# Kernel optimization log

Measured on AMD Instinct MI355X. Metric: run time of the kernel, lower is better.

The kernel has to match this reference:

```python
import jax, jax.numpy as jnp
import numpy as np

B, L, D, NL, VOCAB = 2, 8192, 512, 8, 32
FFT_LEN = 2 * L  # causal linear conv via zero-padded FFT


def layernorm(x, g, b, eps=1e-5):
    mu = jnp.mean(x, axis=-1, keepdims=True)
    var = jnp.var(x, axis=-1, keepdims=True)
    return (x - mu) * jax.lax.rsqrt(var + eps) * g + b


def fftconv(v, h, bias):
    # v: [B, d, L], h: [d, L] long implicit filter, bias: [d] skip (the Hyena 'D' term)
    vf = jnp.fft.rfft(v, n=FFT_LEN)
    hf = jnp.fft.rfft(h, n=FFT_LEN)
    y = jnp.fft.irfft(vf * hf[None], n=FFT_LEN)[..., :L]
    return y + v * bias[:, None]


def short_conv(p, w, b):
    # causal depthwise conv, kernel size 3: p [B, C, L], w [C, 3], b [C]
    pp = jnp.pad(p, ((0, 0), (0, 0), (2, 0)))
    out = jax.lax.conv_general_dilated(pp, w[:, None, :], (1,), 'VALID',
                                       feature_group_count=p.shape[1])
    return out + b[None, :, None]


def setup_inputs() -> dict:
    key = jax.random.key(0)
    ks = jax.random.split(key, 12)
    rn = lambda k, sh, s: jax.random.normal(k, sh, jnp.float32) * s
    d = D
    return {
        'input_ids': jax.random.randint(ks[0], (B, L), 0, VOCAB),
        'emb': rn(ks[1], (VOCAB, d), 0.02),
        'ln1_g': jnp.ones((NL, d)), 'ln1_b': jnp.zeros((NL, d)),
        'Win': rn(ks[2], (NL, d, 3 * d), d ** -0.5), 'bin_': jnp.zeros((NL, 3 * d)),
        'convw': rn(ks[3], (NL, 3 * d, 3), 3 ** -0.5), 'convb': jnp.zeros((NL, 3 * d)),
        'h': rn(ks[4], (NL, d, L), L ** -0.5),  # implicit long filter, materialized
        'Db': rn(ks[5], (NL, d), 1.0),
        'Wout': rn(ks[6], (NL, d, d), d ** -0.5), 'bout': jnp.zeros((NL, d)),
        'ln2_g': jnp.ones((NL, d)), 'ln2_b': jnp.zeros((NL, d)),
        'W1': rn(ks[7], (NL, d, 4 * d), d ** -0.5), 'b1': jnp.zeros((NL, 4 * d)),
        'W2': rn(ks[8], (NL, 4 * d, d), (4 * d) ** -0.5), 'b2': jnp.zeros((NL, d)),
        'lnf_g': jnp.ones((d,)), 'lnf_b': jnp.zeros((d,)),
    }


def reference(input_ids, emb, ln1_g, ln1_b, Win, bin_, convw, convb, h, Db,
              Wout, bout, ln2_g, ln2_b, W1, b1, W2, b2, lnf_g, lnf_b):
    u = emb[input_ids]  # [B, L, d]
    for l in range(NL):  # structural loop over layers
        z = layernorm(u, ln1_g[l], ln1_b[l])
        p = (jnp.einsum('bld,de->ble', z, Win[l]) + bin_[l]).transpose(0, 2, 1)  # [B,3d,L]
        p = short_conv(p, convw[l], convb[l])
        x2, x1, v = jnp.split(p, 3, axis=1)  # each [B, d, L]
        v = fftconv(v * x1, h[l], Db[l])     # gate then FFT long conv (order-2 Hyena)
        y = (v * x2).transpose(0, 2, 1)      # output gate -> [B, L, d]
        u = u + jnp.einsum('bld,de->ble', y, Wout[l]) + bout[l]
        z = layernorm(u, ln2_g[l], ln2_b[l])
        hmid = jax.nn.gelu(jnp.einsum('bld,df->blf', z, W1[l]) + b1[l])
        u = u + jnp.einsum('blf,fd->bld', hmid, W2[l]) + b2[l]
    return layernorm(u, lnf_g, lnf_b)  # last_hidden_state [B, L, d]
```

## Files before the change

### kernel.cpp

```cpp
#include <hip/hip_runtime.h>
#include <hip/hip_bf16.h>
#include <math.h>

#define BB 2
#define LL 8192
#define DD 512
#define NLAYER 8
#define TD 1536
#define HD 2048
#define NFFT 16384
#define NHALF 8192
#define HSTR 4160
#define BLD (BB*LL*DD)
#define BLH ((size_t)BB*LL*HD)

typedef unsigned short u16;
typedef unsigned int   u32;
typedef __bf16 bf16x8 __attribute__((ext_vector_type(8)));
typedef float  f32x4  __attribute__((ext_vector_type(4)));

__device__ __forceinline__ u16 f2bf(float f) {
    union { float f; u32 u; } v; v.f = f;
    u32 r = v.u + 0x7FFF + ((v.u >> 16) & 1);
    return (u16)(r >> 16);
}
__device__ __forceinline__ float bf2f(u16 h) {
    union { u32 u; float f; } v; v.u = (u32)h << 16; return v.f;
}

__device__ __forceinline__ void async_g2l_16(const u16* g, u16* l) {
    __builtin_amdgcn_global_load_lds(
        (const __attribute__((address_space(1))) void*)g,
        (__attribute__((address_space(3))) void*)l,
        16, 0, 0);
}

__device__ __forceinline__ float2 cmul(float2 a, float2 b) {
    return make_float2(a.x * b.x - a.y * b.y, a.x * b.y + a.y * b.x);
}
__device__ __forceinline__ float2 cmulc(float2 a, float2 b) {
    return make_float2(a.x * b.x + a.y * b.y, a.y * b.x - a.x * b.y);
}
__device__ __forceinline__ float2 cadd(float2 a, float2 b) {
    return make_float2(a.x + b.x, a.y + b.y);
}
__device__ __forceinline__ float2 csub(float2 a, float2 b) {
    return make_float2(a.x - b.x, a.y - b.y);
}
__device__ __forceinline__ int drev12(int m) {
    return ((m & 3) << 10) | (((m >> 2) & 3) << 8) | (((m >> 4) & 3) << 6) |
           (((m >> 6) & 3) << 4) | (((m >> 8) & 3) << 2) | ((m >> 10) & 3);
}
__device__ __forceinline__ int perm8k(int k) {
    return ((k & 1) << 12) + drev12(k >> 1);
}
__device__ __forceinline__ int swz(int i) {
    return i ^ (((i >> 4) ^ (i >> 8)) & 15);
}
#define LDX(arr, i) arr[swz(i)]

__global__ void twiddle_kernel(float* twf) {
    int k = blockIdx.x * 256 + threadIdx.x;
    if (k < NFFT) {
        double ang = -2.0 * M_PI * (double)k / (double)NFFT;
        twf[2 * k]     = (float)cos(ang);
        twf[2 * k + 1] = (float)sin(ang);
    }
}

__global__ void embed_kernel(const int* __restrict__ ids,
                             const float* __restrict__ emb,
                             float* __restrict__ u) {
    int i = blockIdx.x * 256 + threadIdx.x;
    if (i < BLD) {
        int row = i >> 9;
        int d   = i & (DD - 1);
        u[i] = emb[ids[row] * DD + d];
    }
}

__global__ __launch_bounds__(256)
void wprep_kernel(const float* __restrict__ W, u16* __restrict__ WtH,
                  u16* __restrict__ WtL, int K, int N, long srcStride, long dstStride) {
    __shared__ float t[64][65];
    const float* src = W + (size_t)blockIdx.z * srcStride;
    u16* dsth = WtH + (size_t)blockIdx.z * dstStride;
    u16* dstl = WtL + (size_t)blockIdx.z * dstStride;
    int n0 = blockIdx.x * 64, k0 = blockIdx.y * 64;
    int tc = threadIdx.x & 63, tr = threadIdx.x >> 6;
    for (int r = tr; r < 64; r += 4)
        t[r][tc] = src[(size_t)(k0 + r) * N + n0 + tc];
    __syncthreads();
    for (int r = tr; r < 64; r += 4) {
        float v = t[tc][r];
        u16 h = f2bf(v);
        dsth[(size_t)(n0 + r) * K + k0 + tc] = h;
        dstl[(size_t)(n0 + r) * K + k0 + tc] = f2bf(v - bf2f(h));
    }
}

template<int MODE>
__global__ __launch_bounds__(128)
void ln_kernel(const float* __restrict__ x, void* __restrict__ out,
               void* __restrict__ outL,
               const float* __restrict__ g, const float* __restrict__ b) {
    int row = blockIdx.x;
    const float4* xr = (const float4*)(x + (size_t)row * DD);
    int t = threadIdx.x;
    float4 v = xr[t];
    float s  = v.x + v.y + v.z + v.w;
    float ss = v.x * v.x + v.y * v.y + v.z * v.z + v.w * v.w;
    for (int off = 32; off; off >>= 1) {
        s  += __shfl_down(s, off);
        ss += __shfl_down(ss, off);
    }
    __shared__ float sm[4];
    if ((t & 63) == 0) { sm[(t >> 6) * 2] = s; sm[(t >> 6) * 2 + 1] = ss; }
    __syncthreads();
    float S = sm[0] + sm[2], SS = sm[1] + sm[3];
    float mu  = S * (1.0f / DD);
    float var = SS * (1.0f / DD) - mu * mu;
    float rs  = rsqrtf(var + 1e-5f);
    float4 gg = ((const float4*)g)[t];
    float4 bb = ((const float4*)b)[t];
    float o[4];
    o[0] = (v.x - mu) * rs * gg.x + bb.x;
    o[1] = (v.y - mu) * rs * gg.y + bb.y;
    o[2] = (v.z - mu) * rs * gg.z + bb.z;
    o[3] = (v.w - mu) * rs * gg.w + bb.w;
    if (MODE == 1) {
        u16 h[4], lo[4];
#pragma unroll
        for (int i = 0; i < 4; i++) {
            h[i]  = f2bf(o[i]);
            lo[i] = f2bf(o[i] - bf2f(h[i]));
        }
        uint2 ph, pl;
        ph.x = (u32)h[0] | ((u32)h[1] << 16);  ph.y = (u32)h[2] | ((u32)h[3] << 16);
        pl.x = (u32)lo[0] | ((u32)lo[1] << 16); pl.y = (u32)lo[2] | ((u32)lo[3] << 16);
        ((uint2*)((u16*)out  + (size_t)row * DD))[t] = ph;
        ((uint2*)((u16*)outL + (size_t)row * DD))[t] = pl;
    } else {
        float4 of = {o[0], o[1], o[2], o[3]};
        ((float4*)((float*)out + (size_t)row * DD))[t] = of;
    }
}

__device__ __forceinline__ float gelu_f(float x) {
    float x3 = x * x * x;
    float t  = tanhf(0.79788456080286541f * (x + 0.044715f * x3));
    return 0.5f * x * (1.0f + t);
}

template<int OUT, bool GELU, int PASSES>
__global__ __launch_bounds__(256)
void mfma_gemm3(const u16* __restrict__ Ah, const u16* __restrict__ Al,
                const u16* __restrict__ Bh, const u16* __restrict__ Bl,
                const float* __restrict__ bias,
                float* __restrict__ Cf, u16* __restrict__ Ch, u16* __restrict__ Cl,
                int M, int N, int K) {
    __shared__ u16 AsH[128 * 32];
    __shared__ u16 AsL[128 * 32];
    __shared__ u16 BsH[128 * 32];
    __shared__ u16 BsL[(PASSES == 3) ? 128 * 32 : 8];
    int nwg  = gridDim.x * gridDim.y;
    int wgid = blockIdx.y * gridDim.x + blockIdx.x;
    int nid  = (wgid & 7) * (nwg >> 3) + (wgid >> 3);
    int bx = nid % gridDim.x, by = nid / gridDim.x;
    int m0 = by * 128, n0 = bx * 128;
    int tid = threadIdx.x;
    int w = tid >> 6, l = tid & 63;
    int wr = w >> 1, wc = w & 1;

    int ch0 = w * 2, ch1 = ch0 + 1;
    size_t offA0 = (size_t)(m0 + ch0 * 16 + (l >> 2)) * K + (l & 3) * 8;
    size_t offA1 = (size_t)(m0 + ch1 * 16 + (l >> 2)) * K + (l & 3) * 8;
    size_t offB0 = (size_t)(n0 + ch0 * 16 + (l >> 2)) * K + (l & 3) * 8;
    size_t offB1 = (size_t)(n0 + ch1 * 16 + (l >> 2)) * K + (l & 3) * 8;

    f32x4 acc[4][4] = {};
    int arow = wr * 64 + (l & 15);
    int brow = wc * 64 + (l & 15);
    int kc   = (l >> 4) * 8;

    for (int k0 = 0; k0 < K; k0 += 32) {
        async_g2l_16(Ah + offA0 + k0, &AsH[ch0 * 512]);
        async_g2l_16(Ah + offA1 + k0, &AsH[ch1 * 512]);
        async_g2l_16(Al + offA0 + k0, &AsL[ch0 * 512]);
        async_g2l_16(Al + offA1 + k0, &AsL[ch1 * 512]);
        async_g2l_16(Bh + offB0 + k0, &BsH[ch0 * 512]);
        async_g2l_16(Bh + offB1 + k0, &BsH[ch1 * 512]);
        if (PASSES == 3) {
            async_g2l_16(Bl + offB0 + k0, &BsL[ch0 * 512]);
            async_g2l_16(Bl + offB1 + k0, &BsL[ch1 * 512]);
        }
        __syncthreads();
        bf16x8 ah[4], al[4], bh[4], bl[4];
#pragma unroll
        for (int i = 0; i < 4; i++) {
            ah[i] = *(const bf16x8*)&AsH[(arow + i * 16) * 32 + kc];
            al[i] = *(const bf16x8*)&AsL[(arow + i * 16) * 32 + kc];
            bh[i] = *(const bf16x8*)&BsH[(brow + i * 16) * 32 + kc];
            if (PASSES == 3)
                bl[i] = *(const bf16x8*)&BsL[(brow + i * 16) * 32 + kc];
        }
#pragma unroll
        for (int mi = 0; mi < 4; mi++)
#pragma unroll
            for (int ni = 0; ni < 4; ni++) {
                acc[mi][ni] = __builtin_amdgcn_mfma_f32_16x16x32_bf16(
                    ah[mi], bh[ni], acc[mi][ni], 0, 0, 0);
                acc[mi][ni] = __builtin_amdgcn_mfma_f32_16x16x32_bf16(
                    al[mi], bh[ni], acc[mi][ni], 0, 0, 0);
                if (PASSES == 3)
                    acc[mi][ni] = __builtin_amdgcn_mfma_f32_16x16x32_bf16(
                        ah[mi], bl[ni], acc[mi][ni], 0, 0, 0);
            }
        __syncthreads();
    }

    int lr = l >> 4, lc = l & 15;
#pragma unroll
    for (int mi = 0; mi < 4; mi++) {
#pragma unroll
        for (int ni = 0; ni < 4; ni++) {
            int col = n0 + wc * 64 + ni * 16 + lc;
            float bv = bias[col];
            int rowb = m0 + wr * 64 + mi * 16 + lr * 4;
#pragma unroll
            for (int r = 0; r < 4; r++) {
                float v = acc[mi][ni][r] + bv;
                if (GELU) v = gelu_f(v);
                size_t off = (size_t)(rowb + r) * N + col;
                if (OUT == 0) {
                    Cf[off] = v;
                } else if (OUT == 1) {
                    u16 h = f2bf(v);
                    Ch[off] = h;
                    Cl[off] = f2bf(v - bf2f(h));
                } else {
                    Cf[off] += v;
                }
            }
        }
    }
}

__global__ __launch_bounds__(256)
void conv_gate_kernel(const float* __restrict__ p, const float* __restrict__ cw,
                      const float* __restrict__ cb, float* __restrict__ vg,
                      float* __restrict__ x2s) {
    __shared__ float tvg[64][65];
    __shared__ float tx2[64][65];
    int b = blockIdx.z, c0 = blockIdx.y * 64, l0 = blockIdx.x * 64;
    int tc = threadIdx.x & 63, tr = threadIdx.x >> 6;
    const float* pb = p + (size_t)b * LL * TD;
    int cx2 = c0 + tc;
    int cx1 = DD + c0 + tc;
    int cv  = 2 * DD + c0 + tc;
    float w20 = cw[cx2 * 3], w21 = cw[cx2 * 3 + 1], w22 = cw[cx2 * 3 + 2], bx2 = cb[cx2];
    float w10 = cw[cx1 * 3], w11 = cw[cx1 * 3 + 1], w12 = cw[cx1 * 3 + 2], bx1 = cb[cx1];
    float wv0 = cw[cv * 3],  wv1 = cw[cv * 3 + 1],  wv2 = cw[cv * 3 + 2],  bv  = cb[cv];
    for (int r = tr; r < 64; r += 4) {
        int l = l0 + r;
        size_t o0 = (size_t)l * TD;
        float p2a = (l >= 2) ? pb[o0 - 2 * TD + cx2] : 0.f;
        float p1a = (l >= 1) ? pb[o0 - TD + cx2] : 0.f;
        float p0a = pb[o0 + cx2];
        float p2b = (l >= 2) ? pb[o0 - 2 * TD + cx1] : 0.f;
        float p1b = (l >= 1) ? pb[o0 - TD + cx1] : 0.f;
        float p0b = pb[o0 + cx1];
        float p2c = (l >= 2) ? pb[o0 - 2 * TD + cv] : 0.f;
        float p1c = (l >= 1) ? pb[o0 - TD + cv] : 0.f;
        float p0c = pb[o0 + cv];
        float x2v = w20 * p2a + w21 * p1a + w22 * p0a + bx2;
        float x1v = w10 * p2b + w11 * p1b + w12 * p0b + bx1;
        float vv  = wv0 * p2c + wv1 * p1c + wv2 * p0c + bv;
        tx2[r][tc] = x2v;
        tvg[r][tc] = vv * x1v;
    }
    __syncthreads();
    for (int r = tr; r < 64; r += 4) {
        size_t o = ((size_t)b * DD + c0 + r) * LL + l0 + tc;
        vg[o]  = tvg[tc][r];
        x2s[o] = tx2[tc][r];
    }
}

__global__ __launch_bounds__(256)
void ytr_kernel(const float* __restrict__ yg, u16* __restrict__ yh,
                u16* __restrict__ yl) {
    __shared__ float t[64][65];
    int b = blockIdx.z, c0 = blockIdx.y * 64, l0 = blockIdx.x * 64;
    int tc = threadIdx.x & 63, tr = threadIdx.x >> 6;
    for (int r = tr; r < 64; r += 4)
        t[r][tc] = yg[((size_t)b * DD + c0 + r) * LL + l0 + tc];
    __syncthreads();
    for (int r = tr; r < 64; r += 4) {
        float v = t[tc][r];
        u16 h = f2bf(v);
        size_t o = ((size_t)(b * LL + l0 + r)) * DD + c0 + tc;
        yh[o] = h;
        yl[o] = f2bf(v - bf2f(h));
    }
}

__device__ __forceinline__ void fft8192_fwd(float2* ld, const float2* __restrict__ tw, int tid) {
    __syncthreads();
    for (int n = tid; n < 4096; n += 1024) {
        float2 a = LDX(ld, n), b = LDX(ld, n + 4096);
        LDX(ld, n) = cadd(a, b);
        float2 d = csub(a, b);
        LDX(ld, n + 4096) = n ? cmul(d, tw[2 * n]) : d;
    }
    for (int s = 0; s < 6; s++) {
        int lm = 12 - 2 * s, lq = lm - 2;
        int Q = 1 << lq;
        __syncthreads();
        for (int g = tid; g < 2048; g += 1024) {
            int half = g >> 10, gg = g & 1023;
            int j = gg & (Q - 1);
            int base = (half << 12) + ((gg >> lq) << lm) + j;
            float2 x0 = LDX(ld, base), x1 = LDX(ld, base + Q);
            float2 x2 = LDX(ld, base + 2 * Q), x3 = LDX(ld, base + 3 * Q);
            float2 a = cadd(x0, x2), b = csub(x0, x2);
            float2 c = cadd(x1, x3), d = csub(x1, x3);
            float2 mid = make_float2(d.y, -d.x);
            float2 u0 = cadd(a, c);
            float2 u1 = cadd(b, mid);
            float2 u2 = csub(a, c);
            float2 u3 = csub(b, mid);
            int e = j << (2 * s);
            if (e) {
                u1 = cmul(u1, tw[4 * e]);
                u2 = cmul(u2, tw[8 * e]);
                u3 = cmul(u3, tw[12 * e]);
            }
            LDX(ld, base) = u0; LDX(ld, base + Q) = u1;
            LDX(ld, base + 2 * Q) = u2; LDX(ld, base + 3 * Q) = u3;
        }
    }
    __syncthreads();
}

__device__ __forceinline__ void fft8192_inv(float2* ld, const float2* __restrict__ tw, int tid) {
    for (int s = 5; s >= 0; s--) {
        int lm = 12 - 2 * s, lq = lm - 2;
        int Q = 1 << lq;
        __syncthreads();
        for (int g = tid; g < 2048; g += 1024) {
            int half = g >> 10, gg = g & 1023;
            int j = gg & (Q - 1);
            int base = (half << 12) + ((gg >> lq) << lm) + j;
            int e = j << (2 * s);
            float2 v0 = LDX(ld, base);
            float2 v1 = LDX(ld, base + Q), v2 = LDX(ld, base + 2 * Q), v3 = LDX(ld, base + 3 * Q);
            if (e) {
                v1 = cmulc(v1, tw[4 * e]);
                v2 = cmulc(v2, tw[8 * e]);
                v3 = cmulc(v3, tw[12 * e]);
            }
            float2 a = cadd(v0, v2), b = csub(v0, v2);
            float2 c = cadd(v1, v3), d = csub(v1, v3);
            float2 id = make_float2(-d.y, d.x);
            LDX(ld, base)         = cadd(a, c);
            LDX(ld, base + Q)     = cadd(b, id);
            LDX(ld, base + 2 * Q) = csub(a, c);
            LDX(ld, base + 3 * Q) = csub(b, id);
        }
    }
    __syncthreads();
    for (int n = tid; n < 4096; n += 1024) {
        float2 a = LDX(ld, n);
        float2 b = LDX(ld, n + 4096);
        if (n) b = cmulc(b, tw[2 * n]);
        LDX(ld, n) = cadd(a, b);
        LDX(ld, n + 4096) = csub(a, b);
    }
    __syncthreads();
}

__global__ __launch_bounds__(1024, 8)
void hf_kernel(const float* __restrict__ h, float2* __restrict__ HfA,
               float2* __restrict__ HfB, const float* __restrict__ twf) {
    __shared__ float2 ld[NHALF];
    int c = blockIdx.x;
    const float2* hp = (const float2*)(h + (size_t)c * LL);
    const float2* tw = (const float2*)twf;
    int tid = threadIdx.x;
    for (int n = tid; n < 4096; n += 1024) LDX(ld, n) = hp[n];
    for (int n = 4096 + tid; n < NHALF; n += 1024) LDX(ld, n) = make_float2(0.f, 0.f);
    fft8192_fwd(ld, tw, tid);
    float2* oa = HfA + (size_t)c * HSTR;
    float2* ob = HfB + (size_t)c * HSTR;
    for (int k = tid; k <= 4096; k += 1024) {
        int kc = (NHALF - k) & (NHALF - 1);
        int p = perm8k(k), pc = perm8k(kc);
        float2 A = LDX(ld, p), B = LDX(ld, pc);
        float2 E = make_float2(0.5f * (A.x + B.x), 0.5f * (A.y - B.y));
        float2 O = make_float2(0.5f * (A.y + B.y), -0.5f * (A.x - B.x));
        float2 t = tw[k];
        float2 tO = cmul(t, O);
        oa[k] = cadd(E, tO);
        ob[k] = csub(E, tO);
    }
}

__global__ __launch_bounds__(1024, 8)
void fftconv_kernel(const float* __restrict__ vg, const float* __restrict__ x2s,
                    const float2* __restrict__ HfA, const float2* __restrict__ HfB,
                    const float* __restrict__ Db, const float* __restrict__ twf,
                    float* __restrict__ yg) {
    __shared__ float2 ld[NHALF];
    int bc = blockIdx.x;
    int c  = bc & (DD - 1);
    const float2* vp  = (const float2*)(vg  + (size_t)bc * LL);
    const float2* x2p = (const float2*)(x2s + (size_t)bc * LL);
    float2*       op  = (float2*)(yg + (size_t)bc * LL);
    const float2* tw = (const float2*)twf;
    int tid = threadIdx.x;
    float2 vv[4];
#pragma unroll
    for (int q = 0; q < 4; q++) {
        int n = tid + q * 1024;
        vv[q] = vp[n];
        LDX(ld, n) = vv[q];
    }
#pragma unroll
    for (int q = 0; q < 4; q++) LDX(ld, tid + 4096 + q * 1024) = make_float2(0.f, 0.f);
    fft8192_fwd(ld, tw, tid);
    const float2* Ha = HfA + (size_t)c * HSTR;
    const float2* Hb = HfB + (size_t)c * HSTR;
    for (int k = tid; k <= 4096; k += 1024) {
        int kc = (NHALF - k) & (NHALF - 1);
        int p = perm8k(k), pc = perm8k(kc);
        float2 A = LDX(ld, p), B = LDX(ld, pc);
        float2 E = make_float2(0.5f * (A.x + B.x), 0.5f * (A.y - B.y));
        float2 O = make_float2(0.5f * (A.y + B.y), -0.5f * (A.x - B.x));
        float2 t = tw[k];
        float2 tO = cmul(t, O);
        float2 X1 = cadd(E, tO);
        float2 X2 = csub(E, tO);
        float2 Hak = Ha[k], Hbk = Hb[k];
        float2 Y1 = cmul(X1, Hak);
        float2 Y2 = cmul(X2, Hbk);
        float2 S  = make_float2(0.5f * (Y1.x + Y2.x), 0.5f * (Y1.y + Y2.y));
        float2 Dd = make_float2(0.5f * (Y1.x - Y2.x), 0.5f * (Y1.y - Y2.y));
        LDX(ld, p) = cadd(S, cmul(make_float2(t.y, t.x), Dd));
        if (kc != k) {
            float2 X1c = make_float2(X2.x, -X2.y);
            float2 X2c = make_float2(X1.x, -X1.y);
            float2 Y1c = cmulc(X1c, Hbk);
            float2 Y2c = cmulc(X2c, Hak);
            float2 Sc = make_float2(0.5f * (Y1c.x + Y2c.x), 0.5f * (Y1c.y + Y2c.y));
            float2 Dc = make_float2(0.5f * (Y1c.x - Y2c.x), 0.5f * (Y1c.y - Y2c.y));
            LDX(ld, pc) = cadd(Sc, cmul(make_float2(t.y, -t.x), Dc));
        }
    }
    fft8192_inv(ld, tw, tid);
    float db = Db[c];
    const float inv = 1.0f / (float)NHALF;
#pragma unroll
    for (int q = 0; q < 4; q++) {
        int n = tid + q * 1024;
        float2 w  = LDX(ld, n);
        float2 xx = x2p[n];
        float y0 = w.x * inv + vv[q].x * db;
        float y1 = w.y * inv + vv[q].y * db;
        op[n] = make_float2(y0 * xx.x, y1 * xx.y);
    }
}

extern "C" void kernel_launch(void* const* d_in, const int* in_sizes, int n_in,
                              void* d_out, int out_size, void* d_ws, size_t ws_size,
                              hipStream_t stream) {
    const int*   ids   = (const int*)  d_in[0];
    const float* emb   = (const float*)d_in[1];
    const float* ln1_g = (const float*)d_in[2];
    const float* ln1_b = (const float*)d_in[3];
    const float* Win   = (const float*)d_in[4];
    const float* bin_  = (const float*)d_in[5];
    const float* convw = (const float*)d_in[6];
    const float* convb = (const float*)d_in[7];
    const float* hflt  = (const float*)d_in[8];
    const float* Db    = (const float*)d_in[9];
    const float* Wout  = (const float*)d_in[10];
    const float* bout  = (const float*)d_in[11];
    const float* ln2_g = (const float*)d_in[12];
    const float* ln2_b = (const float*)d_in[13];
    const float* W1    = (const float*)d_in[14];
    const float* b1    = (const float*)d_in[15];
    const float* W2    = (const float*)d_in[16];
    const float* b2    = (const float*)d_in[17];
    const float* lnf_g = (const float*)d_in[18];
    const float* lnf_b = (const float*)d_in[19];

    char* p_ = (char*)d_ws;
    auto alloc = [&](size_t bytes) {
        char* r = p_; p_ += (bytes + 255) & ~(size_t)255; return r;
    };
    float* u   = (float*)alloc((size_t)BLD * 4);
    u16* zh    = (u16*)  alloc((size_t)BLD * 2);
    u16* zl    = (u16*)  alloc((size_t)BLD * 2);
    char* uni  = alloc(2 * BLH * 2);
    float* pf  = (float*)uni;
    float* yg  = (float*)uni;
    u16* hmh   = (u16*)uni;
    u16* hml   = hmh + BLH;
    float* vg  = (float*)alloc((size_t)BLD * 4);
    float* x2s = (float*)alloc((size_t)BLD * 4);
    u16* yh    = (u16*)  alloc((size_t)BLD * 2);
    u16* yl    = (u16*)  alloc((size_t)BLD * 2);
    float2* HfA = (float2*)alloc((size_t)DD * HSTR * 8);
    float2* HfB = (float2*)alloc((size_t)DD * HSTR * 8);
    float* tw  = (float*)alloc((size_t)2 * NFFT * 4);
    u16* WtInH = (u16*)alloc((size_t)NLAYER * TD * DD * 2);
    u16* WtInL = (u16*)alloc((size_t)NLAYER * TD * DD * 2);
    u16* WtOutH= (u16*)alloc((size_t)NLAYER * DD * DD * 2);
    u16* WtOutL= (u16*)alloc((size_t)NLAYER * DD * DD * 2);
    u16* Wt1H  = (u16*)alloc((size_t)NLAYER * DD * HD * 2);
    u16* Wt1L  = (u16*)alloc((size_t)NLAYER * DD * HD * 2);
    u16* Wt2H  = (u16*)alloc((size_t)NLAYER * HD * DD * 2);
    u16* Wt2L  = (u16*)alloc((size_t)NLAYER * HD * DD * 2);

    twiddle_kernel<<<(NFFT + 255) / 256, 256, 0, stream>>>(tw);
    embed_kernel<<<(BLD + 255) / 256, 256, 0, stream>>>(ids, emb, u);
    wprep_kernel<<<dim3(TD / 64, DD / 64, NLAYER), 256, 0, stream>>>(
        Win, WtInH, WtInL, DD, TD, (long)DD * TD, (long)TD * DD);
    wprep_kernel<<<dim3(DD / 64, DD / 64, NLAYER), 256, 0, stream>>>(
        Wout, WtOutH, WtOutL, DD, DD, (long)DD * DD, (long)DD * DD);
    wprep_kernel<<<dim3(HD / 64, DD / 64, NLAYER), 256, 0, stream>>>(
        W1, Wt1H, Wt1L, DD, HD, (long)DD * HD, (long)DD * HD);
    wprep_kernel<<<dim3(DD / 64, HD / 64, NLAYER), 256, 0, stream>>>(
        W2, Wt2H, Wt2L, HD, DD, (long)HD * DD, (long)HD * DD);

    for (int l = 0; l < NLAYER; l++) {
        ln_kernel<1><<<BB * LL, 128, 0, stream>>>(u, zh, zl,
            ln1_g + l * DD, ln1_b + l * DD);

        mfma_gemm3<0, false, 3><<<dim3(TD / 128, (BB * LL) / 128), 256, 0, stream>>>(
            zh, zl, WtInH + (size_t)l * TD * DD, WtInL + (size_t)l * TD * DD,
            bin_ + (size_t)l * TD, pf, nullptr, nullptr, BB * LL, TD, DD);

        conv_gate_kernel<<<dim3(LL / 64, DD / 64, BB), 256, 0, stream>>>(
            pf, convw + (size_t)l * TD * 3, convb + (size_t)l * TD, vg, x2s);

        hf_kernel<<<DD, 1024, 0, stream>>>(hflt + (size_t)l * DD * LL, HfA, HfB, tw);

        fftconv_kernel<<<BB * DD, 1024, 0, stream>>>(
            vg, x2s, HfA, HfB, Db + (size_t)l * DD, tw, yg);

        ytr_kernel<<<dim3(LL / 64, DD / 64, BB), 256, 0, stream>>>(yg, yh, yl);

        mfma_gemm3<2, false, 2><<<dim3(DD / 128, (BB * LL) / 128), 256, 0, stream>>>(
            yh, yl, WtOutH + (size_t)l * DD * DD, WtOutL + (size_t)l * DD * DD,
            bout + (size_t)l * DD, u, nullptr, nullptr, BB * LL, DD, DD);

        ln_kernel<1><<<BB * LL, 128, 0, stream>>>(u, zh, zl,
            ln2_g + l * DD, ln2_b + l * DD);

        mfma_gemm3<1, true, 2><<<dim3(HD / 128, (BB * LL) / 128), 256, 0, stream>>>(
            zh, zl, Wt1H + (size_t)l * DD * HD, Wt1L + (size_t)l * DD * HD,
            b1 + (size_t)l * HD, nullptr, hmh, hml, BB * LL, HD, DD);

        mfma_gemm3<2, false, 2><<<dim3(DD / 128, (BB * LL) / 128), 256, 0, stream>>>(
            hmh, hml, Wt2H + (size_t)l * HD * DD, Wt2L + (size_t)l * HD * DD,
            b2 + (size_t)l * DD, u, nullptr, nullptr, BB * LL, DD, HD);
    }

    ln_kernel<0><<<BB * LL, 128, 0, stream>>>(u, (float*)d_out, nullptr, lnf_g, lnf_b);
}
```

Measured before the change: 4.731 ms.

## Fuse residual GEMM epilogue with following layernorm over full rows

Adds a GEMM kernel whose block covers 64 full rows of the 512-wide output. It can then add bias and the residual into u, compute the row mean and variance in-block, and write the normalized bf16 hi/lo activations for the next matmul. This replaces the separate ln_kernel launches after the Wout and W2 projections, including the final layernorm. The cost is a new, less tuned GEMM tiling with single-buffered loads and fewer blocks, and a one-pass variance formula.

```diff
diff --git a/kernel.cpp b/kernel.cpp
--- a/kernel.cpp
+++ b/kernel.cpp
@@ -240,6 +240,133 @@
                     Cl[off] = f2bf(v - bf2f(h));
                 } else {
                     Cf[off] += v;
+                }
+            }
+        }
+    }
+}
+
+template<int ZMODE>
+__global__ __launch_bounds__(512)
+void gemm_ln_kernel(const u16* __restrict__ Ah, const u16* __restrict__ Al,
+                    const u16* __restrict__ Bh, const float* __restrict__ bias,
+                    float* __restrict__ u, void* __restrict__ zOut,
+                    void* __restrict__ zOutL, const float* __restrict__ g,
+                    const float* __restrict__ bvec, int K) {
+    __shared__ u16 AsH[64 * 32];
+    __shared__ u16 AsL[64 * 32];
+    __shared__ u16 BsH[512 * 32];
+    __shared__ float redS[64][8];
+    __shared__ float redQ[64][8];
+    __shared__ float2 murs[64];
+    int m0 = blockIdx.x * 64;
+    int tid = threadIdx.x;
+    int w = tid >> 6, l = tid & 63;
+    int lc = l & 15, lr = l >> 4;
+    int kc = lr * 8;
+    int rr = l >> 2, kk = (l & 3) * 8;
+
+    f32x4 acc[4][4] = {};
+    for (int k0 = 0; k0 < K; k0 += 32) {
+#pragma unroll
+        for (int i = 0; i < 5; i++) {
+            int ch = w * 5 + i;
+            if (ch < 4) {
+                async_g2l_16(Ah + (size_t)(m0 + ch * 16 + rr) * K + k0 + kk,
+                             &AsH[ch * 512]);
+            } else if (ch < 8) {
+                async_g2l_16(Al + (size_t)(m0 + (ch - 4) * 16 + rr) * K + k0 + kk,
+                             &AsL[(ch - 4) * 512]);
+            } else {
+                async_g2l_16(Bh + (size_t)((ch - 8) * 16 + rr) * K + k0 + kk,
+                             &BsH[(ch - 8) * 512]);
+            }
+        }
+        __syncthreads();
+        bf16x8 ah[4], al[4], bh[4];
+#pragma unroll
+        for (int i = 0; i < 4; i++) {
+            ah[i] = *(const bf16x8*)&AsH[(i * 16 + lc) * 32 + kc];
+            al[i] = *(const bf16x8*)&AsL[(i * 16 + lc) * 32 + kc];
+            bh[i] = *(const bf16x8*)&BsH[(w * 64 + i * 16 + lc) * 32 + kc];
+        }
+#pragma unroll
+        for (int mi = 0; mi < 4; mi++)
+#pragma unroll
+            for (int ni = 0; ni < 4; ni++) {
+                acc[mi][ni] = __builtin_amdgcn_mfma_f32_16x16x32_bf16(
+                    ah[mi], bh[ni], acc[mi][ni], 0, 0, 0);
+                acc[mi][ni] = __builtin_amdgcn_mfma_f32_16x16x32_bf16(
+                    al[mi], bh[ni], acc[mi][ni], 0, 0, 0);
+            }
+        __syncthreads();
+    }
+
+    float sP[4][4], qP[4][4];
+#pragma unroll
+    for (int mi = 0; mi < 4; mi++)
+#pragma unroll
+        for (int r = 0; r < 4; r++) { sP[mi][r] = 0.f; qP[mi][r] = 0.f; }
+#pragma unroll
+    for (int mi = 0; mi < 4; mi++) {
+#pragma unroll
+        for (int ni = 0; ni < 4; ni++) {
+            int col = w * 64 + ni * 16 + lc;
+            float bv = bias[col];
+#pragma unroll
+            for (int r = 0; r < 4; r++) {
+                int row = mi * 16 + lr * 4 + r;
+                size_t off = (size_t)(m0 + row) * DD + col;
+                float v = (acc[mi][ni][r] + bv) + u[off];
+                u[off] = v;
+                acc[mi][ni][r] = v;
+                sP[mi][r] += v;
+                qP[mi][r] += v * v;
+            }
+        }
+    }
+#pragma unroll
+    for (int m = 1; m < 16; m <<= 1)
+#pragma unroll
+        for (int mi = 0; mi < 4; mi++)
+#pragma unroll
+            for (int r = 0; r < 4; r++) {
+                sP[mi][r] += __shfl_xor(sP[mi][r], m);
+                qP[mi][r] += __shfl_xor(qP[mi][r], m);
+            }
+    {
+        int mi = lc >> 2, r = lc & 3;
+        int row = mi * 16 + lr * 4 + r;
+        redS[row][w] = sP[mi][r];
+        redQ[row][w] = qP[mi][r];
+    }
+    __syncthreads();
+    if (tid < 64) {
+        float S = 0.f, Q = 0.f;
+#pragma unroll
+        for (int ww = 0; ww < 8; ww++) { S += redS[tid][ww]; Q += redQ[tid][ww]; }
+        float mu  = S * (1.0f / DD);
+        float var = Q * (1.0f / DD) - mu * mu;
+        murs[tid] = make_float2(mu, rsqrtf(var + 1e-5f));
+    }
+    __syncthreads();
+#pragma unroll
+    for (int mi = 0; mi < 4; mi++) {
+#pragma unroll
+        for (int r = 0; r < 4; r++) {
+            int row = mi * 16 + lr * 4 + r;
+            float2 mr = murs[row];
+#pragma unroll
+            for (int ni = 0; ni < 4; ni++) {
+                int col = w * 64 + ni * 16 + lc;
+                float z = (acc[mi][ni][r] - mr.x) * mr.y * g[col] + bvec[col];
+                size_t off = (size_t)(m0 + row) * DD + col;
+                if (ZMODE == 1) {
+                    u16 h = f2bf(z);
+                    ((u16*)zOut)[off]  = h;
+                    ((u16*)zOutL)[off] = f2bf(z - bf2f(h));
+                } else {
+                    ((float*)zOut)[off] = z;
                 }
             }
         }
@@ -534,10 +661,9 @@
     wprep_kernel<<<dim3(DD / 64, HD / 64, NLAYER), 256, 0, stream>>>(
         W2, Wt2H, Wt2L, HD, DD, (long)HD * DD, (long)HD * DD);
 
+    ln_kernel<1><<<BB * LL, 128, 0, stream>>>(u, zh, zl, ln1_g, ln1_b);
+
     for (int l = 0; l < NLAYER; l++) {
-        ln_kernel<1><<<BB * LL, 128, 0, stream>>>(u, zh, zl,
-            ln1_g + l * DD, ln1_b + l * DD);
-
         mfma_gemm3<0, false, 3><<<dim3(TD / 128, (BB * LL) / 128), 256, 0, stream>>>(
             zh, zl, WtInH + (size_t)l * TD * DD, WtInL + (size_t)l * TD * DD,
             bin_ + (size_t)l * TD, pf, nullptr, nullptr, BB * LL, TD, DD);
@@ -552,21 +678,22 @@
 
         ytr_kernel<<<dim3(LL / 64, DD / 64, BB), 256, 0, stream>>>(yg, yh, yl);
 
-        mfma_gemm3<2, false, 2><<<dim3(DD / 128, (BB * LL) / 128), 256, 0, stream>>>(
-            yh, yl, WtOutH + (size_t)l * DD * DD, WtOutL + (size_t)l * DD * DD,
-            bout + (size_t)l * DD, u, nullptr, nullptr, BB * LL, DD, DD);
-
-        ln_kernel<1><<<BB * LL, 128, 0, stream>>>(u, zh, zl,
-            ln2_g + l * DD, ln2_b + l * DD);
+        gemm_ln_kernel<1><<<(BB * LL) / 64, 512, 0, stream>>>(
+            yh, yl, WtOutH + (size_t)l * DD * DD, bout + (size_t)l * DD,
+            u, zh, zl, ln2_g + (size_t)l * DD, ln2_b + (size_t)l * DD, DD);
 
         mfma_gemm3<1, true, 2><<<dim3(HD / 128, (BB * LL) / 128), 256, 0, stream>>>(
             zh, zl, Wt1H + (size_t)l * DD * HD, Wt1L + (size_t)l * DD * HD,
             b1 + (size_t)l * HD, nullptr, hmh, hml, BB * LL, HD, DD);
 
-        mfma_gemm3<2, false, 2><<<dim3(DD / 128, (BB * LL) / 128), 256, 0, stream>>>(
-            hmh, hml, Wt2H + (size_t)l * HD * DD, Wt2L + (size_t)l * HD * DD,
-            b2 + (size_t)l * DD, u, nullptr, nullptr, BB * LL, DD, HD);
-    }
-
-    ln_kernel<0><<<BB * LL, 128, 0, stream>>>(u, (float*)d_out, nullptr, lnf_g, lnf_b);
-}
+        if (l < NLAYER - 1) {
+            gemm_ln_kernel<1><<<(BB * LL) / 64, 512, 0, stream>>>(
+                hmh, hml, Wt2H + (size_t)l * HD * DD, b2 + (size_t)l * DD,
+                u, zh, zl, ln1_g + (size_t)(l + 1) * DD, ln1_b + (size_t)(l + 1) * DD, HD);
+        } else {
+            gemm_ln_kernel<0><<<(BB * LL) / 64, 512, 0, stream>>>(
+                hmh, hml, Wt2H + (size_t)l * HD * DD, b2 + (size_t)l * DD,
+                u, d_out, nullptr, lnf_g, lnf_b, HD);
+        }
+    }
+}
```

Result: slower. 5.100 ms (+7.8%).
